# Kernel tuning notes

Measured on AMD Instinct MI355X. Metric: run time of the kernel, lower is better.

The kernel has to match this reference:

```python
import jax, jax.numpy as jnp
import numpy as np

B, D, L = 32, 512, 4096   # batch, latent_dim (dim1), time length
N, D2 = 77, 768           # text tokens, text_latent_dim (dim2)
BC = 24                   # number of conditioned batch elements
H = 8                     # num_heads
EPS = 1e-5


def _layernorm(x, g, b):
    mu = jnp.mean(x, axis=-1, keepdims=True)
    var = jnp.mean(jnp.square(x - mu), axis=-1, keepdims=True)
    return (x - mu) * jax.lax.rsqrt(var + EPS) * g + b


def setup_inputs() -> dict:
    key = jax.random.key(0)
    ks = jax.random.split(key, 8)
    s = 0.02
    return {
        "input_tensor": jax.random.normal(ks[0], (B, D, L), jnp.float32),
        "condition_tensor": jax.random.normal(ks[1], (B, N, D2), jnp.float32),
        "cond_indices": jnp.arange(BC, dtype=jnp.int64 if jax.config.jax_enable_x64 else jnp.int32),
        "ln_g": jnp.ones((D,), jnp.float32),
        "ln_b": jnp.zeros((D,), jnp.float32),
        "tln_g": jnp.ones((D2,), jnp.float32),
        "tln_b": jnp.zeros((D2,), jnp.float32),
        "Wq": jax.random.normal(ks[2], (D, D), jnp.float32) * s,
        "bq": jnp.zeros((D,), jnp.float32),
        "Wk": jax.random.normal(ks[3], (D2, D), jnp.float32) * s,
        "bk": jnp.zeros((D,), jnp.float32),
        "Wv": jax.random.normal(ks[4], (D2, D), jnp.float32) * s,
        "bv": jnp.zeros((D,), jnp.float32),
    }


def reference(input_tensor, condition_tensor, cond_indices,
              ln_g, ln_b, tln_g, tln_b, Wq, bq, Wk, bk, Wv, bv):
    dh = D // H
    # gather conditioned rows; [Bc, D, L] -> [Bc, T=L, D]
    x_cond = jnp.transpose(input_tensor[cond_indices], (0, 2, 1))
    cond = condition_tensor[cond_indices]  # [Bc, N, D2]

    q = _layernorm(x_cond, ln_g, ln_b) @ Wq + bq           # [Bc, T, D]
    cn = _layernorm(cond, tln_g, tln_b)                     # [Bc, N, D2]
    k = (cn @ Wk + bk).reshape(BC, N, H, dh)
    v = (cn @ Wv + bv).reshape(BC, N, H, dh)

    q = jax.nn.softmax(q.reshape(BC, L, H, dh), axis=-1)   # feature-map softmax
    k = jax.nn.softmax(k, axis=1)                           # softmax over tokens N

    context = jnp.einsum('bnhk,bnhv->bhkv', k, v)           # [Bc, H, dh, dh]
    y = jnp.einsum('bthk,bhkv->bthv', q, context).reshape(BC, L, D)

    # scatter residual back: indices are unique, so .add == torch index assignment
    return input_tensor.at[cond_indices].add(jnp.transpose(y, (0, 2, 1)))
```

## Files before the change

### kernel.cpp

```cpp
#include <hip/hip_runtime.h>

#define LN_EPS 1e-5f

typedef __attribute__((ext_vector_type(8))) short bf16x8;
typedef __attribute__((ext_vector_type(4))) float f32x4;

__device__ __forceinline__ unsigned short f2bf(float f){
  unsigned u = __builtin_bit_cast(unsigned, f);
  u = (u + 0x7fffu + ((u >> 16) & 1u)) >> 16;
  return (unsigned short)u;
}
__device__ __forceinline__ float bf2f(unsigned short h){
  unsigned u = ((unsigned)h) << 16;
  return __builtin_bit_cast(float, u);
}
__device__ __forceinline__ unsigned pk2(float lo, float hi){
  return (unsigned)f2bf(lo) | ((unsigned)f2bf(hi) << 16);
}

__global__ void k_aux(const float* __restrict__ Wq, const float* __restrict__ ln_g,
                      const float* __restrict__ ln_b, const float* __restrict__ bq,
                      unsigned short* __restrict__ gWqT, float2* __restrict__ c12,
                      const float* __restrict__ cond, const int* __restrict__ idx,
                      const float* __restrict__ tg, const float* __restrict__ tb,
                      const float* __restrict__ Wk, const float* __restrict__ bk,
                      const float* __restrict__ Wv, const float* __restrict__ bv,
                      float* __restrict__ kbuf, float* __restrict__ vbuf)
{
  __shared__ float cn[16][768];
  const int tid = threadIdx.x;

  if(blockIdx.z == 24){
    const int pb = blockIdx.x + 4*blockIdx.y;
    if(pb >= 8) return;
    float* const r1 = &cn[0][0];
    float* const r2 = &cn[0][0] + 256;
    const int n0 = pb * 64;
    const int c = tid & 63, q = tid >> 6;
    const int n = n0 + c;
    float c1p = 0.f, c2p = 0.f;
    for(int i=0;i<128;i+=4){
      ushort4 pkv;
      unsigned short* pp = (unsigned short*)&pkv;
      #pragma unroll
      for(int j=0;j<4;j++){
        const int d = q*128 + i + j;
        const float wv = Wq[(size_t)d*512 + n];
        const unsigned short hb = f2bf(ln_g[d] * wv);
        pp[j] = hb;
        c2p += bf2f(hb);
        c1p += ln_b[d] * wv;
      }
      *(ushort4*)(gWqT + (size_t)n*512 + q*128 + i) = pkv;
    }
    r1[c*4 + q] = c1p; r2[c*4 + q] = c2p;
    __syncthreads();
    if(q == 0){
      float a = 0.f, b2 = 0.f;
      #pragma unroll
      for(int j=0;j<4;j++){ a += r1[c*4+j]; b2 += r2[c*4+j]; }
      c12[n] = make_float2(a + bq[n], b2);
    }
    return;
  }

  const int bc = blockIdx.z, nc = blockIdx.y, dc = blockIdx.x;
  const int b = idx[bc];
  const int n0 = nc * 16;
  int nrows = 77 - n0; if(nrows > 16) nrows = 16;
  const int w = tid >> 6, lane = tid & 63;

  for(int r = w; r < nrows; r += 4){
    const float* src = cond + ((size_t)b * 77 + n0 + r) * 768;
    float vals[12]; float s1 = 0.f, s2 = 0.f;
    #pragma unroll
    for(int i=0;i<12;i++){ float x = src[lane + i*64]; vals[i]=x; s1+=x; s2+=x*x; }
    #pragma unroll
    for(int off=1; off<64; off<<=1){ s1 += __shfl_xor(s1, off); s2 += __shfl_xor(s2, off); }
    const float mu  = s1 * (1.f/768.f);
    const float var = s2 * (1.f/768.f) - mu*mu;
    const float rs  = rsqrtf(var + LN_EPS);
    #pragma unroll
    for(int i=0;i<12;i++){ const int c2 = lane + i*64; cn[r][c2] = (vals[i]-mu)*rs*tg[c2] + tb[c2]; }
  }
  __syncthreads();

  const int dq = tid & 63;
  const int part = tid >> 6;
  const float* W    = (dc < 2) ? Wk : Wv;
  const float* bias = (dc < 2) ? bk : bv;
  float* obuf       = (dc < 2) ? kbuf : vbuf;
  const int d0 = (dc & 1) * 256 + dq * 4;

  float acc[4][4] = {};
  for(int i=0;i<768;i++){
    const float4 wv = *(const float4*)(W + (size_t)i * 512 + d0);
    #pragma unroll
    for(int j=0;j<4;j++){
      const float c = cn[part*4 + j][i];
      acc[j][0] += c * wv.x; acc[j][1] += c * wv.y;
      acc[j][2] += c * wv.z; acc[j][3] += c * wv.w;
    }
  }
  #pragma unroll
  for(int j=0;j<4;j++){
    const int r = part*4 + j, n = n0 + r;
    if(r < nrows){
      float4 o;
      o.x = acc[j][0] + bias[d0+0];
      o.y = acc[j][1] + bias[d0+1];
      o.z = acc[j][2] + bias[d0+2];
      o.w = acc[j][3] + bias[d0+3];
      *(float4*)(obuf + ((size_t)bc * 77 + n) * 512 + d0) = o;
    }
  }
}

__global__ void k_ctx(const float* __restrict__ kbuf, const float* __restrict__ vbuf,
                      unsigned short* __restrict__ ctxP)
{
  __shared__ float kk[77][64];
  __shared__ float vv[77][64];
  __shared__ float inv_s[64];
  const int h = blockIdx.x, bc = blockIdx.y;
  const int tid = threadIdx.x;
  for(int e = tid; e < 77*64; e += 256){
    const int n = e >> 6, c = e & 63;
    kk[n][c] = kbuf[((size_t)bc * 77 + n) * 512 + h*64 + c];
    vv[n][c] = vbuf[((size_t)bc * 77 + n) * 512 + h*64 + c];
  }
  __syncthreads();
  if(tid < 64){
    float m = -1e30f;
    for(int n=0;n<77;n++) m = fmaxf(m, kk[n][tid]);
    float s = 0.f;
    for(int n=0;n<77;n++){ const float e = __expf(kk[n][tid] - m); kk[n][tid] = e; s += e; }
    inv_s[tid] = 1.f / s;
  }
  __syncthreads();
  #pragma unroll
  for(int j=0;j<16;j++){
    const int o = tid + 256*j;
    const int v = o >> 6, k2 = o & 63;
    float a = 0.f;
    for(int n=0;n<77;n++) a += kk[n][k2] * vv[n][v];
    const int pos = ((((k2>>5)*4 + (v>>4))*4 + ((k2>>3)&3))*16 + (v&15))*8 + (k2&7);
    ctxP[((size_t)(bc*8 + h)) * 4096 + pos] = f2bf(a * inv_s[k2]);
  }
}

__global__ __launch_bounds__(256, 3)
void k_fused(const float* __restrict__ input, const int* __restrict__ idx,
             const unsigned short* __restrict__ gWqT, const float2* __restrict__ c12,
             const unsigned short* __restrict__ ctxP, float* __restrict__ out)
{
  const int nt  = blockIdx.x;
  const int by  = blockIdx.y;
  const int tid = threadIdx.x;

  if(by >= 1536){
    const int cid = (by - 1536)*2 + nt;
    const int nb = cid >> 6, chunk = cid & 63;
    int cnt = 0, bsel = 0;
    for(int b2 = 0; b2 < 32; ++b2){
      bool member = false;
      #pragma unroll
      for(int i2 = 0; i2 < 24; ++i2) member |= (idx[i2] == b2);
      if(!member){ if(cnt == nb) bsel = b2; ++cnt; }
    }
    const float4* s = (const float4*)(input + (size_t)bsel * 2097152) + chunk*8192;
    float4*       d = (float4*)      (out   + (size_t)bsel * 2097152) + chunk*8192;
    #pragma unroll
    for(int i = 0; i < 32; ++i) d[i*256 + tid] = s[i*256 + tid];
    return;
  }

  __shared__ __align__(16) char smem[40960];
  unsigned short* const P = (unsigned short*)smem;
  float* const mu_s = (float*)(smem + 36864);
  float* const rs_s = (float*)(smem + 37120);
  float* const red1 = (float*)(smem + 37376);
  float* const red2 = (float*)(smem + 38400);

  const int lane = tid & 63, w = tid >> 6;
  const int col = lane & 15, g = lane >> 4;
  const int bc = by >> 6, b = idx[bc];
  const int t0 = (by & 63) * 64;
  const int nbase = nt * 256;
  const float* xb = input + (size_t)b * 2097152;

  const int t = tid & 63;
  const int q = tid >> 6;
  const float* xcol = xb + t0 + t;

  const int wxA = t*128 + ((((q<<1)    ) ^ ((t>>1)&7)) << 4);
  const int wxB = t*128 + ((((q<<1) | 1) ^ ((t>>1)&7)) << 4);

  int offA[2][4];
  #pragma unroll
  for(int kk=0; kk<2; ++kk)
    #pragma unroll
    for(int mt=0; mt<4; ++mt){
      const int row = mt*16 + col;
      offA[kk][mt] = row*128 + (((kk*4 + g) ^ ((row>>1)&7)) << 4);
    }

  const char* wrow[4];
  #pragma unroll
  for(int ntl=0; ntl<4; ++ntl)
    wrow[ntl] = (const char*)gWqT + (size_t)(nbase + w*64 + ntl*16 + col)*1024 + g*16;

  float s1 = 0.f, s2 = 0.f;
  f32x4 acc[4][4] = {};

  #define XLOAD(xv, ks)                                                       \
  { _Pragma("unroll")                                                         \
    for(int j=0;j<16;j++) xv[j] = xcol[(size_t)((ks)*64 + q*16 + j) * 4096]; }
  #define XSTAT(xv)                                                           \
  { _Pragma("unroll")                                                         \
    for(int j=0;j<16;j++){ s1 += xv[j]; s2 += xv[j]*xv[j]; } }
  #define XPUT(xv, Xd)                                                        \
  { uint4 ua, ub;                                                             \
    ua.x = pk2(xv[0],xv[1]);  ua.y = pk2(xv[2],xv[3]);                        \
    ua.z = pk2(xv[4],xv[5]);  ua.w = pk2(xv[6],xv[7]);                        \
    ub.x = pk2(xv[8],xv[9]);  ub.y = pk2(xv[10],xv[11]);                      \
    ub.z = pk2(xv[12],xv[13]);ub.w = pk2(xv[14],xv[15]);                      \
    *(uint4*)((Xd) + wxA) = ua;                                               \
    *(uint4*)((Xd) + wxB) = ub; }

  {
    float xv[16];
    XLOAD(xv, 0);
    XSTAT(xv);
    XPUT(xv, smem);
  }
  asm volatile("s_waitcnt lgkmcnt(0)" ::: "memory");
  __builtin_amdgcn_s_barrier();

  for(int ks = 0; ks < 8; ++ks){
    char* const Xc = smem + ((ks & 1) << 13);
    char* const Xn = smem + (((ks + 1) & 1) << 13);

    float xn[16];
    if(ks < 7){ XLOAD(xn, ks+1); }
    bf16x8 wf[2][4];
    #pragma unroll
    for(int kk=0; kk<2; ++kk)
      #pragma unroll
      for(int ntl=0; ntl<4; ++ntl)
        wf[kk][ntl] = *(const bf16x8*)(wrow[ntl] + ks*128 + kk*64);

    #pragma unroll
    for(int kk=0; kk<2; ++kk){
      bf16x8 af[4];
      #pragma unroll
      for(int mt=0; mt<4; ++mt) af[mt] = *(const bf16x8*)(Xc + offA[kk][mt]);
      #pragma unroll
      for(int ntl=0; ntl<4; ++ntl)
        #pragma unroll
        for(int mt=0; mt<4; ++mt)
          acc[mt][ntl] = __builtin_amdgcn_mfma_f32_16x16x32_bf16(af[mt], wf[kk][ntl], acc[mt][ntl], 0, 0, 0);
    }

    __builtin_amdgcn_s_barrier();

    if(ks < 7){
      XSTAT(xn);
      XPUT(xn, Xn);
      asm volatile("s_waitcnt lgkmcnt(0)" ::: "memory");
      __builtin_amdgcn_s_barrier();
    }
  }
  #undef XLOAD
  #undef XSTAT
  #undef XPUT

  red1[t*4 + q] = s1;
  red2[t*4 + q] = s2;
  __syncthreads();
  if(tid < 64){
    const float a  = red1[tid*4] + red1[tid*4+1] + red1[tid*4+2] + red1[tid*4+3];
    const float c2 = red2[tid*4] + red2[tid*4+1] + red2[tid*4+2] + red2[tid*4+3];
    const float mu  = a * (1.f/512.f);
    const float var = c2 * (1.f/512.f) - mu*mu;
    mu_s[tid] = mu;
    rs_s[tid] = rsqrtf(var + LN_EPS);
  }
  __syncthreads();

  const int head = nt*4 + w;
  float c1b[4], c2v[4];
  #pragma unroll
  for(int ntl=0; ntl<4; ++ntl){
    const float2 cc = c12[nbase + w*64 + ntl*16 + col];
    c1b[ntl] = cc.x;
    c2v[ntl] = cc.y;
  }
  #pragma unroll
  for(int mt=0; mt<4; ++mt){
    #pragma unroll
    for(int r=0; r<4; ++r){
      const int tl = mt*16 + g*4 + r;
      const float rsr = rs_s[tl];
      const float mrc = rsr * mu_s[tl];
      float v[4];
      #pragma unroll
      for(int ntl=0; ntl<4; ++ntl)
        v[ntl] = rsr*acc[mt][ntl][r] - mrc*c2v[ntl] + c1b[ntl];
      float m = fmaxf(fmaxf(v[0],v[1]), fmaxf(v[2],v[3]));
      m = fmaxf(m, __shfl_xor(m, 1));
      m = fmaxf(m, __shfl_xor(m, 2));
      m = fmaxf(m, __shfl_xor(m, 4));
      m = fmaxf(m, __shfl_xor(m, 8));
      float s = 0.f;
      #pragma unroll
      for(int ntl=0; ntl<4; ++ntl){ v[ntl] = __expf(v[ntl] - m); s += v[ntl]; }
      s += __shfl_xor(s, 1);
      s += __shfl_xor(s, 2);
      s += __shfl_xor(s, 4);
      s += __shfl_xor(s, 8);
      const float inv = 1.f / s;
      #pragma unroll
      for(int ntl=0; ntl<4; ++ntl) acc[mt][ntl][r] = v[ntl] * inv;
    }
  }

  unsigned short* const Pw = P + w * (64*72);
  #pragma unroll
  for(int mt=0; mt<4; ++mt)
    #pragma unroll
    for(int ntl=0; ntl<4; ++ntl)
      #pragma unroll
      for(int r=0; r<4; ++r)
        Pw[(mt*16 + g*4 + r)*72 + ntl*16 + col] = f2bf(acc[mt][ntl][r]);

  const unsigned short* cp = ctxP + (size_t)(bc*8 + head) * 4096;
  f32x4 y[4][4] = {};
  #pragma unroll
  for(int ks2=0; ks2<2; ++ks2){
    bf16x8 pa[4];
    #pragma unroll
    for(int mt=0; mt<4; ++mt)
      pa[mt] = *(const bf16x8*)(Pw + (mt*16 + col)*72 + ks2*32 + g*8);
    bf16x8 cv[4];
    #pragma unroll
    for(int vt=0; vt<4; ++vt)
      cv[vt] = *(const bf16x8*)(cp + (size_t)(((ks2*4 + vt)*4 + g)*16 + col) * 8);
    #pragma unroll
    for(int mt=0; mt<4; ++mt)
      #pragma unroll
      for(int vt=0; vt<4; ++vt)
        y[mt][vt] = __builtin_amdgcn_mfma_f32_16x16x32_bf16(pa[mt], cv[vt], y[mt][vt], 0, 0, 0);
  }

  float* const ob = out + (size_t)b * 2097152;
  #pragma unroll
  for(int mt=0; mt<4; ++mt)
    #pragma unroll
    for(int vt=0; vt<4; ++vt){
      const size_t a = (size_t)(head*64 + vt*16 + col)*4096
                     + (size_t)(t0 + mt*16 + g*4);
      const float4 xr4 = *(const float4*)(xb + a);
      float4 o4;
      o4.x = xr4.x + y[mt][vt][0];
      o4.y = xr4.y + y[mt][vt][1];
      o4.z = xr4.z + y[mt][vt][2];
      o4.w = xr4.w + y[mt][vt][3];
      *(float4*)(ob + a) = o4;
    }
}

extern "C" void kernel_launch(void* const* d_in, const int* in_sizes, int n_in,
                              void* d_out, int out_size, void* d_ws, size_t ws_size,
                              hipStream_t stream)
{
  const float* input = (const float*)d_in[0];
  const float* cond  = (const float*)d_in[1];
  const int*   idx   = (const int*)d_in[2];
  const float* ln_g  = (const float*)d_in[3];
  const float* ln_b  = (const float*)d_in[4];
  const float* tln_g = (const float*)d_in[5];
  const float* tln_b = (const float*)d_in[6];
  const float* Wq    = (const float*)d_in[7];
  const float* bq    = (const float*)d_in[8];
  const float* Wk    = (const float*)d_in[9];
  const float* bk    = (const float*)d_in[10];
  const float* Wv    = (const float*)d_in[11];
  const float* bv    = (const float*)d_in[12];
  float* out = (float*)d_out;
  char*  ws  = (char*)d_ws;

  unsigned short* gWqT = (unsigned short*)(ws);
  float2*         c12  = (float2*)(ws + 524288);
  unsigned short* ctxP = (unsigned short*)(ws + 528384);
  float* kbuf = (float*)(ws + 2101248);
  float* vbuf = (float*)(ws + 2101248 + 3784704);

  k_aux  <<<dim3(4,5,25),  dim3(256), 0, stream>>>(Wq, ln_g, ln_b, bq, gWqT, c12,
                                                   cond, idx, tln_g, tln_b,
                                                   Wk, bk, Wv, bv, kbuf, vbuf);
  k_ctx  <<<dim3(8,24),    dim3(256), 0, stream>>>(kbuf, vbuf, ctxP);
  k_fused<<<dim3(2,1792),  dim3(256), 0, stream>>>(input, idx, gWqT, c12, ctxP, out);
}
```

Before: 425.7 us.

## Stage full 64x512 bf16 X tile in LDS with vectorized loads before GEMM

Replaces the double-buffered, scalar-load k-step pipeline with a single up-front phase. All 512 channels for 64 timesteps are loaded with float4 reads, LayerNorm statistics are accumulated via shuffles, and the whole bf16 tile (64 KB) is written to LDS. The Q GEMM then runs from LDS without per-step barriers, and the P buffer uses an XOR swizzle. This removes the scalar strided loads and the many barriers, but raises LDS use to about 68 KB, cuts occupancy from 3 to 2 blocks, and drops the overlap of loads with MFMA.

```diff
diff --git a/kernel.cpp b/kernel.cpp
--- a/kernel.cpp
+++ b/kernel.cpp
@@ -13,9 +13,6 @@
 __device__ __forceinline__ float bf2f(unsigned short h){
   unsigned u = ((unsigned)h) << 16;
   return __builtin_bit_cast(float, u);
-}
-__device__ __forceinline__ unsigned pk2(float lo, float hi){
-  return (unsigned)f2bf(lo) | ((unsigned)f2bf(hi) << 16);
 }
 
 __global__ void k_aux(const float* __restrict__ Wq, const float* __restrict__ ln_g,
@@ -149,10 +146,10 @@
   }
 }
 
-__global__ __launch_bounds__(256, 3)
-void k_fused(const float* __restrict__ input, const int* __restrict__ idx,
-             const unsigned short* __restrict__ gWqT, const float2* __restrict__ c12,
-             const unsigned short* __restrict__ ctxP, float* __restrict__ out)
+__global__ __launch_bounds__(256, 2)
+void k_fuse(const float* __restrict__ input, const int* __restrict__ idx,
+            const unsigned short* __restrict__ gWqT, const float2* __restrict__ c12,
+            const unsigned short* __restrict__ ctxP, float* __restrict__ out)
 {
   const int nt  = blockIdx.x;
   const int by  = blockIdx.y;
@@ -175,12 +172,11 @@
     return;
   }
 
-  __shared__ __align__(16) char smem[40960];
-  unsigned short* const P = (unsigned short*)smem;
-  float* const mu_s = (float*)(smem + 36864);
-  float* const rs_s = (float*)(smem + 37120);
-  float* const red1 = (float*)(smem + 37376);
-  float* const red2 = (float*)(smem + 38400);
+  __shared__ __align__(16) char smem[68096];
+  float* const red1 = (float*)(smem + 65536);
+  float* const red2 = (float*)(smem + 66560);
+  float* const mu_s = (float*)(smem + 67584);
+  float* const rs_s = (float*)(smem + 67840);
 
   const int lane = tid & 63, w = tid >> 6;
   const int col = lane & 15, g = lane >> 4;
@@ -189,94 +185,40 @@
   const int nbase = nt * 256;
   const float* xb = input + (size_t)b * 2097152;
 
-  const int t = tid & 63;
-  const int q = tid >> 6;
-  const float* xcol = xb + t0 + t;
-
-  const int wxA = t*128 + ((((q<<1)    ) ^ ((t>>1)&7)) << 4);
-  const int wxB = t*128 + ((((q<<1) | 1) ^ ((t>>1)&7)) << 4);
-
-  int offA[2][4];
-  #pragma unroll
-  for(int kk=0; kk<2; ++kk)
-    #pragma unroll
-    for(int mt=0; mt<4; ++mt){
-      const int row = mt*16 + col;
-      offA[kk][mt] = row*128 + (((kk*4 + g) ^ ((row>>1)&7)) << 4);
-    }
-
-  const char* wrow[4];
-  #pragma unroll
-  for(int ntl=0; ntl<4; ++ntl)
-    wrow[ntl] = (const char*)gWqT + (size_t)(nbase + w*64 + ntl*16 + col)*1024 + g*16;
-
-  float s1 = 0.f, s2 = 0.f;
-  f32x4 acc[4][4] = {};
-
-  #define XLOAD(xv, ks)                                                       \
-  { _Pragma("unroll")                                                         \
-    for(int j=0;j<16;j++) xv[j] = xcol[(size_t)((ks)*64 + q*16 + j) * 4096]; }
-  #define XSTAT(xv)                                                           \
-  { _Pragma("unroll")                                                         \
-    for(int j=0;j<16;j++){ s1 += xv[j]; s2 += xv[j]*xv[j]; } }
-  #define XPUT(xv, Xd)                                                        \
-  { uint4 ua, ub;                                                             \
-    ua.x = pk2(xv[0],xv[1]);  ua.y = pk2(xv[2],xv[3]);                        \
-    ua.z = pk2(xv[4],xv[5]);  ua.w = pk2(xv[6],xv[7]);                        \
-    ub.x = pk2(xv[8],xv[9]);  ub.y = pk2(xv[10],xv[11]);                      \
-    ub.z = pk2(xv[12],xv[13]);ub.w = pk2(xv[14],xv[15]);                      \
-    *(uint4*)((Xd) + wxA) = ua;                                               \
-    *(uint4*)((Xd) + wxB) = ub; }
-
-  {
-    float xv[16];
-    XLOAD(xv, 0);
-    XSTAT(xv);
-    XPUT(xv, smem);
-  }
-  asm volatile("s_waitcnt lgkmcnt(0)" ::: "memory");
-  __builtin_amdgcn_s_barrier();
-
-  for(int ks = 0; ks < 8; ++ks){
-    char* const Xc = smem + ((ks & 1) << 13);
-    char* const Xn = smem + (((ks + 1) & 1) << 13);
-
-    float xn[16];
-    if(ks < 7){ XLOAD(xn, ks+1); }
-    bf16x8 wf[2][4];
-    #pragma unroll
-    for(int kk=0; kk<2; ++kk)
-      #pragma unroll
-      for(int ntl=0; ntl<4; ++ntl)
-        wf[kk][ntl] = *(const bf16x8*)(wrow[ntl] + ks*128 + kk*64);
-
-    #pragma unroll
-    for(int kk=0; kk<2; ++kk){
-      bf16x8 af[4];
-      #pragma unroll
-      for(int mt=0; mt<4; ++mt) af[mt] = *(const bf16x8*)(Xc + offA[kk][mt]);
-      #pragma unroll
-      for(int ntl=0; ntl<4; ++ntl)
-        #pragma unroll
-        for(int mt=0; mt<4; ++mt)
-          acc[mt][ntl] = __builtin_amdgcn_mfma_f32_16x16x32_bf16(af[mt], wf[kk][ntl], acc[mt][ntl], 0, 0, 0);
-    }
-
-    __builtin_amdgcn_s_barrier();
-
-    if(ks < 7){
-      XSTAT(xn);
-      XPUT(xn, Xn);
-      asm volatile("s_waitcnt lgkmcnt(0)" ::: "memory");
-      __builtin_amdgcn_s_barrier();
-    }
-  }
-  #undef XLOAD
-  #undef XSTAT
-  #undef XPUT
-
-  red1[t*4 + q] = s1;
-  red2[t*4 + q] = s2;
+  const int tq = tid & 15;
+  const int dq = tid >> 4;
+  const float* xcol = xb + t0 + tq*4;
+
+  float s1[4] = {0,0,0,0}, s2[4] = {0,0,0,0};
+  #pragma unroll 2
+  for(int p = 0; p < 8; ++p){
+    const int d0 = p*64 + dq*4;
+    float4 xr[4];
+    #pragma unroll
+    for(int di=0; di<4; ++di) xr[di] = *(const float4*)(xcol + (size_t)(d0+di)*4096);
+    #pragma unroll
+    for(int j=0; j<4; ++j){
+      const float v0 = (&xr[0].x)[j], v1 = (&xr[1].x)[j];
+      const float v2 = (&xr[2].x)[j], v3 = (&xr[3].x)[j];
+      s1[j] += v0+v1+v2+v3;
+      s2[j] += v0*v0 + v1*v1 + v2*v2 + v3*v3;
+      const int t = tq*4 + j;
+      const int byteo = t*1024 + ((((d0>>3) ^ (t&7)))<<4) + ((d0&7)<<1);
+      *(ushort4*)(smem + byteo) = make_ushort4(f2bf(v0), f2bf(v1), f2bf(v2), f2bf(v3));
+    }
+  }
+  #pragma unroll
+  for(int j=0;j<4;j++){
+    s1[j] += __shfl_xor(s1[j], 16); s2[j] += __shfl_xor(s2[j], 16);
+    s1[j] += __shfl_xor(s1[j], 32); s2[j] += __shfl_xor(s2[j], 32);
+  }
+  if(lane < 16){
+    #pragma unroll
+    for(int j=0;j<4;j++){
+      red1[(lane*4 + j)*4 + w] = s1[j];
+      red2[(lane*4 + j)*4 + w] = s2[j];
+    }
+  }
   __syncthreads();
   if(tid < 64){
     const float a  = red1[tid*4] + red1[tid*4+1] + red1[tid*4+2] + red1[tid*4+3];
@@ -287,6 +229,34 @@
     rs_s[tid] = rsqrtf(var + LN_EPS);
   }
   __syncthreads();
+
+  int rowp[4], row7[4];
+  #pragma unroll
+  for(int mt=0; mt<4; ++mt){
+    const int row = mt*16 + col;
+    rowp[mt] = row*1024;
+    row7[mt] = row & 7;
+  }
+  const char* wrow[4];
+  #pragma unroll
+  for(int ntl=0; ntl<4; ++ntl)
+    wrow[ntl] = (const char*)gWqT + (size_t)(nbase + w*64 + ntl*16 + col)*1024 + g*16;
+
+  f32x4 acc[4][4] = {};
+  #pragma unroll 4
+  for(int ks=0; ks<16; ++ks){
+    bf16x8 wf[4], af[4];
+    #pragma unroll
+    for(int ntl=0; ntl<4; ++ntl) wf[ntl] = *(const bf16x8*)(wrow[ntl] + ks*64);
+    #pragma unroll
+    for(int mt=0; mt<4; ++mt)
+      af[mt] = *(const bf16x8*)(smem + rowp[mt] + (((ks*4 + g) ^ row7[mt]) << 4));
+    #pragma unroll
+    for(int mt=0; mt<4; ++mt)
+      #pragma unroll
+      for(int ntl=0; ntl<4; ++ntl)
+        acc[mt][ntl] = __builtin_amdgcn_mfma_f32_16x16x32_bf16(af[mt], wf[ntl], acc[mt][ntl], 0, 0, 0);
+  }
 
   const int head = nt*4 + w;
   float c1b[4], c2v[4];
@@ -325,14 +295,20 @@
     }
   }
 
-  unsigned short* const Pw = P + w * (64*72);
+  __syncthreads();
+
+  char* const Pw = smem + w * 8192;
   #pragma unroll
   for(int mt=0; mt<4; ++mt)
     #pragma unroll
     for(int ntl=0; ntl<4; ++ntl)
       #pragma unroll
-      for(int r=0; r<4; ++r)
-        Pw[(mt*16 + g*4 + r)*72 + ntl*16 + col] = f2bf(acc[mt][ntl][r]);
+      for(int r=0; r<4; ++r){
+        const int row = mt*16 + g*4 + r;
+        const int k   = ntl*16 + col;
+        const int byteo = row*128 + ((((k>>3) ^ (row&7)))<<4) + ((k&7)<<1);
+        *(unsigned short*)(Pw + byteo) = f2bf(acc[mt][ntl][r]);
+      }
 
   const unsigned short* cp = ctxP + (size_t)(bc*8 + head) * 4096;
   f32x4 y[4][4] = {};
@@ -340,8 +316,10 @@
   for(int ks2=0; ks2<2; ++ks2){
     bf16x8 pa[4];
     #pragma unroll
-    for(int mt=0; mt<4; ++mt)
-      pa[mt] = *(const bf16x8*)(Pw + (mt*16 + col)*72 + ks2*32 + g*8);
+    for(int mt=0; mt<4; ++mt){
+      const int row = mt*16 + col;
+      pa[mt] = *(const bf16x8*)(Pw + row*128 + ((((ks2*4 + g) ^ (row&7)))<<4));
+    }
     bf16x8 cv[4];
     #pragma unroll
     for(int vt=0; vt<4; ++vt)
@@ -396,9 +374,9 @@
   float* kbuf = (float*)(ws + 2101248);
   float* vbuf = (float*)(ws + 2101248 + 3784704);
 
-  k_aux  <<<dim3(4,5,25),  dim3(256), 0, stream>>>(Wq, ln_g, ln_b, bq, gWqT, c12,
-                                                   cond, idx, tln_g, tln_b,
-                                                   Wk, bk, Wv, bv, kbuf, vbuf);
-  k_ctx  <<<dim3(8,24),    dim3(256), 0, stream>>>(kbuf, vbuf, ctxP);
-  k_fused<<<dim3(2,1792),  dim3(256), 0, stream>>>(input, idx, gWqT, c12, ctxP, out);
-}
+  k_aux <<<dim3(4,5,25),  dim3(256), 0, stream>>>(Wq, ln_g, ln_b, bq, gWqT, c12,
+                                                  cond, idx, tln_g, tln_b,
+                                                  Wk, bk, Wv, bv, kbuf, vbuf);
+  k_ctx <<<dim3(8,24),    dim3(256), 0, stream>>>(kbuf, vbuf, ctxP);
+  k_fuse<<<dim3(2,1792),  dim3(256), 0, stream>>>(input, idx, gWqT, c12, ctxP, out);
+}
```

Result: slower. 439.5 us (+3.2%).
